# Kernel tuning notes

Hardware: AMD Instinct MI355X
Metric: run time of the kernel (lower is better)

Reference implementation:

```python
import jax, jax.numpy as jnp
import numpy as np

N = 2048        # batch (nodes/edges)
DIM = 512       # irreps dim for x, y, and output
C = 16          # channel multiplicity
NNZ = 4096      # number of sparse CG paths


def setup_inputs() -> dict:
    key = jax.random.key(0)
    k1, k2, k3, k4, k5, k6 = jax.random.split(key, 6)
    x = jax.random.normal(k1, (N, DIM, C), dtype=jnp.float32)
    y = jax.random.normal(k2, (N, DIM, C), dtype=jnp.float32)
    scale = jax.random.normal(k3, (NNZ,), dtype=jnp.float32)
    index1 = jax.random.randint(k4, (NNZ,), 0, DIM)
    index2 = jax.random.randint(k5, (NNZ,), 0, DIM)
    index_out = jnp.sort(jax.random.randint(k6, (NNZ,), 0, DIM))
    return {"x": x, "y": y, "scale": scale,
            "index1": index1, "index2": index2, "index_out": index_out,
            "out_size": DIM}


def reference(x, y, scale, index1, index2, index_out, out_size):
    # gather both operands along the irreps dim  -> [N, NNZ, C]
    inter = scale[None, :, None] * x[:, index1, :] * y[:, index2, :]
    # scatter-add (segment + scatter in the original, fused here since
    # segment-then-scatter over disjoint segments == one scatter-add)
    out = jnp.zeros((x.shape[0], out_size, x.shape[-1]), dtype=x.dtype)
    out = out.at[:, index_out, :].add(inter)  # [N, out_size, C]
    return out
```

## Files before the change

### kernel.cpp

```cpp
#include <hip/hip_runtime.h>

constexpr int DIM = 512;
constexpr int C   = 16;
constexpr int TPB = 1024;

__global__ void seg_starts_kernel(const int* __restrict__ io,
                                  int* __restrict__ start,
                                  int nnz, int dim) {
    int d = blockIdx.x * blockDim.x + threadIdx.x;
    if (d > dim) return;
    int lo = 0, hi = nnz;
    while (lo < hi) {
        int mid = (lo + hi) >> 1;
        if (io[mid] < d) lo = mid + 1; else hi = mid;
    }
    start[d] = lo;
}

__global__ __launch_bounds__(TPB) void tp_lds_kernel(
    const float* __restrict__ x, const float* __restrict__ y,
    const float* __restrict__ scale,
    const int* __restrict__ i1, const int* __restrict__ i2,
    const int* __restrict__ start,
    float* __restrict__ out) {
    __shared__ float xs[DIM * C];
    __shared__ float ys[DIM * C];

    const int n = blockIdx.x;
    const float4* __restrict__ xr = reinterpret_cast<const float4*>(x + (size_t)n * (DIM * C));
    const float4* __restrict__ yr = reinterpret_cast<const float4*>(y + (size_t)n * (DIM * C));
    float4* xs4 = reinterpret_cast<float4*>(xs);
    float4* ys4 = reinterpret_cast<float4*>(ys);

    #pragma unroll
    for (int i = threadIdx.x; i < DIM * C / 4; i += TPB) {
        xs4[i] = xr[i];
        ys4[i] = yr[i];
    }
    __syncthreads();

    const int c4   = (threadIdx.x & 3) << 2;
    const int dloc = threadIdx.x >> 2;
    float* __restrict__ orow = out + (size_t)n * (DIM * C);

    #pragma unroll
    for (int db = 0; db < DIM; db += TPB / 4) {
        const int d = db + dloc;
        const int s = start[d];
        const int e = start[d + 1];
        float ax = 0.f, ay = 0.f, az = 0.f, aw = 0.f;
        for (int p = s; p < e; ++p) {
            const int   a  = i1[p];
            const int   b  = i2[p];
            const float sc = scale[p];
            const float4 xv = *reinterpret_cast<const float4*>(xs + a * C + c4);
            const float4 yv = *reinterpret_cast<const float4*>(ys + b * C + c4);
            ax = fmaf(sc * xv.x, yv.x, ax);
            ay = fmaf(sc * xv.y, yv.y, ay);
            az = fmaf(sc * xv.z, yv.z, az);
            aw = fmaf(sc * xv.w, yv.w, aw);
        }
        *reinterpret_cast<float4*>(orow + d * C + c4) = make_float4(ax, ay, az, aw);
    }
}

extern "C" void kernel_launch(void* const* d_in, const int* in_sizes, int n_in,
                              void* d_out, int out_size, void* d_ws, size_t ws_size,
                              hipStream_t stream) {
    const float* x     = (const float*)d_in[0];
    const float* y     = (const float*)d_in[1];
    const float* scale = (const float*)d_in[2];
    const int*   i1    = (const int*)d_in[3];
    const int*   i2    = (const int*)d_in[4];
    const int*   io    = (const int*)d_in[5];
    float* out = (float*)d_out;

    const int nnz = in_sizes[2];
    const int N   = in_sizes[0] / (DIM * C);

    int* start = (int*)d_ws;

    seg_starts_kernel<<<(DIM + 1 + 255) / 256, 256, 0, stream>>>(io, start, nnz, DIM);
    tp_lds_kernel<<<N, TPB, 0, stream>>>(x, y, scale, i1, i2, start, out);
}
```

Measured before the change: 66.48 us.

## Pack path metadata, swizzle LDS rows, and software-pipeline the gather loop

A setup kernel now packs i1, i2 and scale into one int4 per path, with the LDS offsets precomputed in XOR-swizzled form. The main kernel stores x and y rows in LDS with an XOR swizzle on the float4 slot, meant to spread the random-row float4 reads across banks. The per-path loop is software-pipelined, so the next path's metadata and LDS operands are loaded before the current FMAs. The cost is an extra int4 workspace array, 16 bytes per path, placed at a fixed 4096-byte offset, and a few more registers per thread.

```diff
diff --git a/kernel.cpp b/kernel.cpp
--- a/kernel.cpp
+++ b/kernel.cpp
@@ -4,24 +4,34 @@
 constexpr int C   = 16;
 constexpr int TPB = 1024;
 
-__global__ void seg_starts_kernel(const int* __restrict__ io,
-                                  int* __restrict__ start,
-                                  int nnz, int dim) {
-    int d = blockIdx.x * blockDim.x + threadIdx.x;
-    if (d > dim) return;
-    int lo = 0, hi = nnz;
-    while (lo < hi) {
-        int mid = (lo + hi) >> 1;
-        if (io[mid] < d) lo = mid + 1; else hi = mid;
+__device__ __forceinline__ int swz_base(int a) { return (a << 4) ^ ((a & 7) << 2); }
+
+__global__ void setup_kernel(const int* __restrict__ io,
+                             const int* __restrict__ i1,
+                             const int* __restrict__ i2,
+                             const float* __restrict__ scale,
+                             int* __restrict__ start,
+                             int4* __restrict__ pdata,
+                             int nnz) {
+    int t = blockIdx.x * blockDim.x + threadIdx.x;
+    if (t < nnz) {
+        int a = i1[t], b = i2[t];
+        pdata[t] = make_int4(swz_base(a), swz_base(b), __float_as_int(scale[t]), 0);
     }
-    start[d] = lo;
+    if (t <= DIM) {
+        int lo = 0, hi = nnz;
+        while (lo < hi) {
+            int mid = (lo + hi) >> 1;
+            if (io[mid] < t) lo = mid + 1; else hi = mid;
+        }
+        start[t] = lo;
+    }
 }
 
 __global__ __launch_bounds__(TPB) void tp_lds_kernel(
     const float* __restrict__ x, const float* __restrict__ y,
-    const float* __restrict__ scale,
-    const int* __restrict__ i1, const int* __restrict__ i2,
     const int* __restrict__ start,
+    const int4* __restrict__ pdata,
     float* __restrict__ out) {
     __shared__ float xs[DIM * C];
     __shared__ float ys[DIM * C];
@@ -34,8 +44,10 @@
 
     #pragma unroll
     for (int i = threadIdx.x; i < DIM * C / 4; i += TPB) {
-        xs4[i] = xr[i];
-        ys4[i] = yr[i];
+        const int a = i >> 2, cq = i & 3;
+        const int slot = ((a << 2) ^ (a & 7)) ^ cq;
+        xs4[slot] = xr[i];
+        ys4[slot] = yr[i];
     }
     __syncthreads();
 
@@ -49,12 +61,23 @@
         const int s = start[d];
         const int e = start[d + 1];
         float ax = 0.f, ay = 0.f, az = 0.f, aw = 0.f;
-        for (int p = s; p < e; ++p) {
-            const int   a  = i1[p];
-            const int   b  = i2[p];
-            const float sc = scale[p];
-            const float4 xv = *reinterpret_cast<const float4*>(xs + a * C + c4);
-            const float4 yv = *reinterpret_cast<const float4*>(ys + b * C + c4);
+        int p = s;
+        if (p < e) {
+            int4   pd = pdata[p];
+            float4 xv = *reinterpret_cast<const float4*>(xs + (pd.x ^ c4));
+            float4 yv = *reinterpret_cast<const float4*>(ys + (pd.y ^ c4));
+            while (++p < e) {
+                const int4   pdn = pdata[p];
+                const float4 xvn = *reinterpret_cast<const float4*>(xs + (pdn.x ^ c4));
+                const float4 yvn = *reinterpret_cast<const float4*>(ys + (pdn.y ^ c4));
+                const float sc = __int_as_float(pd.z);
+                ax = fmaf(sc * xv.x, yv.x, ax);
+                ay = fmaf(sc * xv.y, yv.y, ay);
+                az = fmaf(sc * xv.z, yv.z, az);
+                aw = fmaf(sc * xv.w, yv.w, aw);
+                pd = pdn; xv = xvn; yv = yvn;
+            }
+            const float sc = __int_as_float(pd.z);
             ax = fmaf(sc * xv.x, yv.x, ax);
             ay = fmaf(sc * xv.y, yv.y, ay);
             az = fmaf(sc * xv.z, yv.z, az);
@@ -78,8 +101,11 @@
     const int nnz = in_sizes[2];
     const int N   = in_sizes[0] / (DIM * C);
 
-    int* start = (int*)d_ws;
+    int*  start = (int*)d_ws;
+    int4* pdata = (int4*)((char*)d_ws + 4096);
 
-    seg_starts_kernel<<<(DIM + 1 + 255) / 256, 256, 0, stream>>>(io, start, nnz, DIM);
-    tp_lds_kernel<<<N, TPB, 0, stream>>>(x, y, scale, i1, i2, start, out);
+    const int setup_threads = (nnz > DIM + 1 ? nnz : DIM + 1);
+    setup_kernel<<<(setup_threads + 255) / 256, 256, 0, stream>>>(
+        io, i1, i2, scale, start, pdata, nnz);
+    tp_lds_kernel<<<N, TPB, 0, stream>>>(x, y, start, pdata, out);
 }
```

Result: slower. 102.9 us (+54.7%).
